# Kernel optimization log

Measured on AMD Instinct MI355X. Metric: run time of the kernel, lower is better.

Reference implementation:

```python
import jax, jax.numpy as jnp
import numpy as np

K = 3            # TAGConv default number of hops
NUM_GRAPHS = 128 # graphs in the batch (for global_add_pool)


def _gcn_norm(src, dst, n):
    # PyG gcn_norm (symmetric, no self-loops): w_e = d[src]^-1/2 * d[dst]^-1/2
    deg = jnp.zeros((n,), jnp.float32).at[dst].add(1.0)
    dinv = jnp.where(deg > 0, jax.lax.rsqrt(deg), 0.0)
    return dinv[src] * dinv[dst]


def _tagconv(x, src, dst, wn, W, b):
    # out = sum_{k=0..K} (norm_adj^k x) @ W[k] + b
    n = x.shape[0]
    h = x
    out = h @ W[0]
    for k in range(1, K + 1):
        h = jax.ops.segment_sum(h[src] * wn[:, None], dst, num_segments=n)
        out = out + h @ W[k]
    return out + b


def setup_inputs() -> dict:
    key = jax.random.key(0)
    ks = jax.random.split(key, 8)
    N, E, D, H = 50000, 800000, 64, 64
    x = jax.random.normal(ks[0], (N, D), jnp.float32)
    edge_index = jax.random.randint(ks[1], (2, E), 0, N, dtype=jnp.int32)
    batch_ids = jnp.sort(jax.random.randint(ks[2], (N,), 0, NUM_GRAPHS, dtype=jnp.int32))
    def glorot(k, sh):
        return jax.random.normal(k, sh, jnp.float32) / np.float32(np.sqrt(sh[-2]))
    W0 = glorot(ks[3], (K + 1, D, H)); b0 = jnp.zeros((H,), jnp.float32)
    W1 = glorot(ks[4], (K + 1, H, H)); b1 = jnp.zeros((H,), jnp.float32)
    alpha0 = jnp.full((1,), 0.25, jnp.float32)  # PReLU default init
    alpha1 = jnp.full((1,), 0.25, jnp.float32)
    Wout = glorot(ks[5], (H, 1)); bout = jnp.zeros((1,), jnp.float32)
    return dict(x=x, edge_index=edge_index, batch_ids=batch_ids,
                W0=W0, b0=b0, W1=W1, b1=b1,
                alpha0=alpha0, alpha1=alpha1, Wout=Wout, bout=bout)


def reference(x, edge_index, batch_ids, W0, b0, W1, b1, alpha0, alpha1, Wout, bout):
    src, dst = edge_index[0], edge_index[1]
    wn = _gcn_norm(src, dst, x.shape[0])
    # layer 0: TAGConv -> (dropout=identity in eval) -> PReLU
    h = _tagconv(x, src, dst, wn, W0, b0)
    h = jnp.where(h >= 0, h, alpha0 * h)
    # layer 1
    h = _tagconv(h, src, dst, wn, W1, b1)
    h = jnp.where(h >= 0, h, alpha1 * h)
    # global_add_pool over graphs, then linear critic head
    g = jax.ops.segment_sum(h, batch_ids, num_segments=NUM_GRAPHS)  # [G, H]
    return g @ Wout + bout  # [G, 1]
```

## Files before the change

kernel.cpp:

```cpp
#include <hip/hip_runtime.h>
#include <hip/hip_bf16.h>
#include <hip/hip_fp16.h>

#define D 64
#define GRAPHS 128

using bf16x8 = __attribute__((ext_vector_type(8))) short;
using f32x4  = __attribute__((ext_vector_type(4))) float;


__device__ __forceinline__ float bf2f(unsigned short u) {
    return __uint_as_float(((unsigned)u) << 16);
}
__device__ __forceinline__ unsigned short f2bf(float f) {
    unsigned u = __float_as_uint(f);
    unsigned r = (u + 0x7FFFu + ((u >> 16) & 1u)) >> 16;
    return (unsigned short)r;
}


__global__ void deg_prep_kernel(const int* __restrict__ dst, int* __restrict__ deg,
                                int* __restrict__ pos, int E, int EB4,
                                const float* __restrict__ W0, const float* __restrict__ W1,
                                unsigned short* __restrict__ WF0, unsigned short* __restrict__ WF1,
                                const float* __restrict__ x, unsigned short* __restrict__ H, int NH) {
    int b = blockIdx.x;
    if (b < EB4) {
        int e0 = (b * 256 + threadIdx.x) * 4;
        if (e0 + 4 <= E) {
            int4 d4 = *(const int4*)(dst + e0);
            int4 p;
            p.x = atomicAdd(&deg[d4.x], 1);
            p.y = atomicAdd(&deg[d4.y], 1);
            p.z = atomicAdd(&deg[d4.z], 1);
            p.w = atomicAdd(&deg[d4.w], 1);
            *(int4*)(pos + e0) = p;
        } else {
            for (int e = e0; e < E; ++e) pos[e] = atomicAdd(&deg[dst[e]], 1);
        }
    } else if (b < EB4 + 128) {
        int idx = (b - EB4) * 256 + threadIdx.x;
        int i = idx & 16383;
        int j = i & 7, lane = (i >> 3) & 63, ct = (i >> 9) & 3, kt = i >> 11;
        int n = ct * 16 + (lane & 15);
        int k = kt * 32 + (lane >> 4) * 8 + j;
        if (idx < 16384) WF0[i] = f2bf(W0[k * 64 + n]);
        else             WF1[i] = f2bf(W1[k * 64 + n]);
    } else {
        int i = (b - EB4 - 128) * 256 + threadIdx.x;
        if (i < NH) {
            int n = i >> 3, f = (i & 7) * 8;
            float4 x0 = *(const float4*)(x + (size_t)n * 64 + f);
            float4 x1 = *(const float4*)(x + (size_t)n * 64 + f + 4);
            bf16x8 pk;
            pk[0] = f2bf(x0.x); pk[1] = f2bf(x0.y); pk[2] = f2bf(x0.z); pk[3] = f2bf(x0.w);
            pk[4] = f2bf(x1.x); pk[5] = f2bf(x1.y); pk[6] = f2bf(x1.z); pk[7] = f2bf(x1.w);
            *(bf16x8*)(H + (size_t)n * 256 + f) = pk;
        }
    }
}


__global__ void scan_all_kernel(const int* __restrict__ deg, float* __restrict__ dinv,
                                int* __restrict__ pdeg, int* __restrict__ rowstart,
                                unsigned int* __restrict__ ep, int* __restrict__ total, int N) {
    __shared__ int s[256];
    __shared__ int base_sh;
    int i = blockIdx.x * 256 + threadIdx.x;
    int d = 0, p = 0;
    if (i < N) {
        d = deg[i];
        dinv[i] = d > 0 ? rsqrtf((float)d) : 0.0f;
        p = (d + 7) & ~7;
        pdeg[i] = p;
    }
    s[threadIdx.x] = p;
    __syncthreads();
    for (int st = 1; st < 256; st <<= 1) {
        int add = (threadIdx.x >= st) ? s[threadIdx.x - st] : 0;
        __syncthreads();
        s[threadIdx.x] += add;
        __syncthreads();
    }
    if (threadIdx.x == 255) base_sh = atomicAdd(total, s[255]);
    __syncthreads();
    if (i < N) {
        int excl = base_sh + s[threadIdx.x] - p;
        rowstart[i] = excl;
        for (int q = excl + d; q < excl + p; ++q) ep[q] = 0u;
    }
}


__global__ void scatter_kernel(const int* __restrict__ src, const int* __restrict__ dst,
                               const int* __restrict__ pos, const float* __restrict__ dinv,
                               const int* __restrict__ rowstart, unsigned int* __restrict__ ep, int E) {
    int e0 = (blockIdx.x * 256 + threadIdx.x) * 4;
    if (e0 + 4 <= E) {
        int4 s4 = *(const int4*)(src + e0);
        int4 d4 = *(const int4*)(dst + e0);
        int4 p4 = *(const int4*)(pos + e0);
        float v0 = dinv[s4.x], v1 = dinv[s4.y], v2 = dinv[s4.z], v3 = dinv[s4.w];
        int r0 = rowstart[d4.x], r1 = rowstart[d4.y], r2 = rowstart[d4.z], r3 = rowstart[d4.w];
        ep[r0 + p4.x] = (unsigned)s4.x | ((unsigned)__half_as_ushort(__float2half(v0)) << 16);
        ep[r1 + p4.y] = (unsigned)s4.y | ((unsigned)__half_as_ushort(__float2half(v1)) << 16);
        ep[r2 + p4.z] = (unsigned)s4.z | ((unsigned)__half_as_ushort(__float2half(v2)) << 16);
        ep[r3 + p4.w] = (unsigned)s4.w | ((unsigned)__half_as_ushort(__float2half(v3)) << 16);
    } else {
        for (int e = e0; e < E; ++e) {
            int dd = dst[e], ss = src[e];
            ep[rowstart[dd] + pos[e]] = (unsigned)ss | ((unsigned)__half_as_ushort(__float2half(dinv[ss])) << 16);
        }
    }
}


#define GROWS 8

__global__ __launch_bounds__(512, 8)
void gather_kernel(const unsigned short* __restrict__ in,
                   unsigned short* __restrict__ out,
                   const int* __restrict__ rowstart, const int* __restrict__ pdeg,
                   const float* __restrict__ dinv, const unsigned int* __restrict__ ep, int N) {
    int wid = blockIdx.x * GROWS + (threadIdx.x >> 6);
    if (wid >= N) return;
    int lane = threadIdx.x & 63;
    int g  = lane >> 3;
    int fl = (lane & 7) * 8;

    int start = __builtin_amdgcn_readfirstlane(rowstart[wid]);
    int cnt   = __builtin_amdgcn_readfirstlane(pdeg[wid]);
    float dd  = dinv[wid];

    float a0=0.f,a1=0.f,a2=0.f,a3=0.f,a4=0.f,a5=0.f,a6=0.f,a7=0.f;
    float c0=0.f,c1=0.f,c2=0.f,c3=0.f,c4=0.f,c5=0.f,c6=0.f,c7=0.f;
    unsigned eA = 0, eB = 0;
    if (cnt > 0) {
        eA = ep[start + g];
        eB = (8 < cnt) ? ep[start + 8 + g] : 0u;
    }
    for (int i = 0; i < cnt; i += 16) {
        unsigned cA = eA, cB = eB;
        if (i + 16 < cnt) {
            eA = ep[start + i + 16 + g];
            eB = (i + 24 < cnt) ? ep[start + i + 24 + g] : 0u;
        }
        bf16x8 rA = *(const bf16x8*)(in + (size_t)(cA & 0xFFFFu) * 256 + fl);
        bf16x8 rB = *(const bf16x8*)(in + (size_t)(cB & 0xFFFFu) * 256 + fl);
        float wA = __half2float(__ushort_as_half((unsigned short)(cA >> 16)));
        float wB = __half2float(__ushort_as_half((unsigned short)(cB >> 16)));
        a0 = fmaf(wA, bf2f((unsigned short)rA[0]), a0);
        a1 = fmaf(wA, bf2f((unsigned short)rA[1]), a1);
        a2 = fmaf(wA, bf2f((unsigned short)rA[2]), a2);
        a3 = fmaf(wA, bf2f((unsigned short)rA[3]), a3);
        a4 = fmaf(wA, bf2f((unsigned short)rA[4]), a4);
        a5 = fmaf(wA, bf2f((unsigned short)rA[5]), a5);
        a6 = fmaf(wA, bf2f((unsigned short)rA[6]), a6);
        a7 = fmaf(wA, bf2f((unsigned short)rA[7]), a7);
        c0 = fmaf(wB, bf2f((unsigned short)rB[0]), c0);
        c1 = fmaf(wB, bf2f((unsigned short)rB[1]), c1);
        c2 = fmaf(wB, bf2f((unsigned short)rB[2]), c2);
        c3 = fmaf(wB, bf2f((unsigned short)rB[3]), c3);
        c4 = fmaf(wB, bf2f((unsigned short)rB[4]), c4);
        c5 = fmaf(wB, bf2f((unsigned short)rB[5]), c5);
        c6 = fmaf(wB, bf2f((unsigned short)rB[6]), c6);
        c7 = fmaf(wB, bf2f((unsigned short)rB[7]), c7);
    }
    a0 += c0; a1 += c1; a2 += c2; a3 += c3;
    a4 += c4; a5 += c5; a6 += c6; a7 += c7;
    a0 += __shfl_xor(a0, 8, 64); a0 += __shfl_xor(a0, 16, 64); a0 += __shfl_xor(a0, 32, 64);
    a1 += __shfl_xor(a1, 8, 64); a1 += __shfl_xor(a1, 16, 64); a1 += __shfl_xor(a1, 32, 64);
    a2 += __shfl_xor(a2, 8, 64); a2 += __shfl_xor(a2, 16, 64); a2 += __shfl_xor(a2, 32, 64);
    a3 += __shfl_xor(a3, 8, 64); a3 += __shfl_xor(a3, 16, 64); a3 += __shfl_xor(a3, 32, 64);
    a4 += __shfl_xor(a4, 8, 64); a4 += __shfl_xor(a4, 16, 64); a4 += __shfl_xor(a4, 32, 64);
    a5 += __shfl_xor(a5, 8, 64); a5 += __shfl_xor(a5, 16, 64); a5 += __shfl_xor(a5, 32, 64);
    a6 += __shfl_xor(a6, 8, 64); a6 += __shfl_xor(a6, 16, 64); a6 += __shfl_xor(a6, 32, 64);
    a7 += __shfl_xor(a7, 8, 64); a7 += __shfl_xor(a7, 16, 64); a7 += __shfl_xor(a7, 32, 64);
    if (g == 0) {
        bf16x8 pk;
        pk[0] = f2bf(a0 * dd); pk[1] = f2bf(a1 * dd);
        pk[2] = f2bf(a2 * dd); pk[3] = f2bf(a3 * dd);
        pk[4] = f2bf(a4 * dd); pk[5] = f2bf(a5 * dd);
        pk[6] = f2bf(a6 * dd); pk[7] = f2bf(a7 * dd);
        *(bf16x8*)(out + (size_t)wid * 256 + fl) = pk;
    }
}


#define LROW 72

template<int MODE>
__global__ __launch_bounds__(256, 4)
void tag_gemm_kernel(const unsigned short* __restrict__ H,
                     const unsigned short* __restrict__ Wfrag,
                     const float* __restrict__ bias, const float* __restrict__ alpha,
                     const float* __restrict__ Wout, const int* __restrict__ batch,
                     const float* __restrict__ bout,
                     unsigned short* __restrict__ H2, float* __restrict__ outp, int N) {
    __shared__ float bins[GRAPHS];
    __shared__ unsigned short lbuf[64 * LROW];
    if (MODE == 3) {
        if (threadIdx.x < GRAPHS) bins[threadIdx.x] = 0.0f;
        __syncthreads();
    }
    if (MODE == 2) {
        if (blockIdx.x == 0 && threadIdx.x < GRAPHS) outp[threadIdx.x] = bout[0];
    }

    int w = threadIdx.x >> 6, lane = threadIdx.x & 63;
    int m = lane & 15, quad = lane >> 4;
    int rowbase = blockIdx.x * 64 + w * 16;
    int arow = rowbase + m;
    size_t aoff = (size_t)min(arow, N - 1) * 256 + quad * 8;

    f32x4 acc0 = {0.f, 0.f, 0.f, 0.f}, acc1 = acc0, acc2 = acc0, acc3 = acc0;
#pragma unroll
    for (int kt = 0; kt < 8; ++kt) {
        bf16x8 A = *(const bf16x8*)(H + aoff + kt * 32);
        const unsigned short* wf = Wfrag + ((size_t)(kt * 4) * 64 + lane) * 8;
        bf16x8 B0 = *(const bf16x8*)(wf + 0 * 64 * 8);
        bf16x8 B1 = *(const bf16x8*)(wf + 1 * 64 * 8);
        bf16x8 B2 = *(const bf16x8*)(wf + 2 * 64 * 8);
        bf16x8 B3 = *(const bf16x8*)(wf + 3 * 64 * 8);
        acc0 = __builtin_amdgcn_mfma_f32_16x16x32_bf16(A, B0, acc0, 0, 0, 0);
        acc1 = __builtin_amdgcn_mfma_f32_16x16x32_bf16(A, B1, acc1, 0, 0, 0);
        acc2 = __builtin_amdgcn_mfma_f32_16x16x32_bf16(A, B2, acc2, 0, 0, 0);
        acc3 = __builtin_amdgcn_mfma_f32_16x16x32_bf16(A, B3, acc3, 0, 0, 0);
    }

    float al = alpha[0];
    f32x4 accs[4] = {acc0, acc1, acc2, acc3};
    if (MODE == 2) {
#pragma unroll
        for (int ct = 0; ct < 4; ++ct) {
            int col = ct * 16 + m;
            float b = bias[col];
#pragma unroll
            for (int r = 0; r < 4; ++r) {
                int lrow = w * 16 + quad * 4 + r;
                float v = accs[ct][r] + b;
                v = v >= 0.f ? v : al * v;
                lbuf[lrow * LROW + col] = f2bf(v);
            }
        }
        __syncthreads();
#pragma unroll
        for (int k = 0; k < 2; ++k) {
            int c = threadIdx.x * 2 + k;
            int lrow = c >> 3, part = c & 7;
            int grow = blockIdx.x * 64 + lrow;
            if (grow < N) {
                bf16x8 pk = *(const bf16x8*)(lbuf + lrow * LROW + part * 8);
                *(bf16x8*)(H2 + (size_t)grow * 256 + part * 8) = pk;
            }
        }
    } else {
        float rv0 = 0.f, rv1 = 0.f, rv2 = 0.f, rv3 = 0.f;
#pragma unroll
        for (int ct = 0; ct < 4; ++ct) {
            int col = ct * 16 + m;
            float b = bias[col], wo = Wout[col];
            float v;
            v = accs[ct][0] + b; v = v >= 0.f ? v : al * v; rv0 = fmaf(v, wo, rv0);
            v = accs[ct][1] + b; v = v >= 0.f ? v : al * v; rv1 = fmaf(v, wo, rv1);
            v = accs[ct][2] + b; v = v >= 0.f ? v : al * v; rv2 = fmaf(v, wo, rv2);
            v = accs[ct][3] + b; v = v >= 0.f ? v : al * v; rv3 = fmaf(v, wo, rv3);
        }
        float rv[4] = {rv0, rv1, rv2, rv3};
#pragma unroll
        for (int r = 0; r < 4; ++r) {
            float v = rv[r];
            v += __shfl_xor(v, 8, 16);
            v += __shfl_xor(v, 4, 16);
            v += __shfl_xor(v, 2, 16);
            v += __shfl_xor(v, 1, 16);
            int row = rowbase + quad * 4 + r;
            if (m == 0 && row < N) atomicAdd(&bins[batch[row]], v);
        }
        __syncthreads();
        if (threadIdx.x < GRAPHS) {
            float bv = bins[threadIdx.x];
            if (bv != 0.0f) atomicAdd(&outp[threadIdx.x], bv);
        }
    }
}

extern "C" void kernel_launch(void* const* d_in, const int* in_sizes, int n_in,
                              void* d_out, int out_size, void* d_ws, size_t ws_size,
                              hipStream_t stream) {
    const float* x     = (const float*)d_in[0];
    const int*   ei    = (const int*)d_in[1];
    const int*   batch = (const int*)d_in[2];
    const float* W0    = (const float*)d_in[3];
    const float* b0    = (const float*)d_in[4];
    const float* W1    = (const float*)d_in[5];
    const float* b1    = (const float*)d_in[6];
    const float* a0    = (const float*)d_in[7];
    const float* a1    = (const float*)d_in[8];
    const float* Wout  = (const float*)d_in[9];
    const float* bout  = (const float*)d_in[10];

    const int N = in_sizes[0] / D;
    const int E = in_sizes[1] / 2;
    const int* src = ei;
    const int* dst = ei + E;

    size_t off = 0;
    auto alloc = [&](size_t bytes) -> void* {
        void* p = (char*)d_ws + off;
        off = (off + bytes + 255) & ~(size_t)255;
        return p;
    };
    const int NB = (N + 255) / 256;
    int*   deg      = (int*)alloc((size_t)(N + 1) * 4);
    int*   pdeg     = (int*)alloc((size_t)N * 4);
    int*   rowstart = (int*)alloc((size_t)N * 4);
    float* dinv     = (float*)alloc((size_t)N * 4);
    int*   pos      = (int*)alloc((size_t)E * 4);
    unsigned int* epack = (unsigned int*)alloc(((size_t)E + 8ull * N) * 4);
    unsigned short* HA = (unsigned short*)alloc((size_t)N * 256 * 2);
    unsigned short* HB = (unsigned short*)alloc((size_t)N * 256 * 2);
    unsigned short* WF0 = (unsigned short*)alloc(16384 * 2);
    unsigned short* WF1 = (unsigned short*)alloc(16384 * 2);

    const int EB4 = (E + 1023) / 1024;
    const int NXH = (N * 8 + 255) / 256;
    const int NG = (N + GROWS - 1) / GROWS;
    const int NM = (N + 63) / 64;

    hipMemsetAsync(deg, 0, (size_t)(N + 1) * 4, stream);
    deg_prep_kernel<<<EB4 + 128 + NXH, 256, 0, stream>>>(dst, deg, pos, E, EB4,
                                                         W0, W1, WF0, WF1, x, HA, N * 8);
    scan_all_kernel<<<NB, 256, 0, stream>>>(deg, dinv, pdeg, rowstart, epack, deg + N, N);
    scatter_kernel<<<EB4, 256, 0, stream>>>(src, dst, pos, dinv, rowstart, epack, E);

    gather_kernel<<<NG, 512, 0, stream>>>(HA + 0 * 64, HA + 1 * 64, rowstart, pdeg, dinv, epack, N);
    gather_kernel<<<NG, 512, 0, stream>>>(HA + 1 * 64, HA + 2 * 64, rowstart, pdeg, dinv, epack, N);
    gather_kernel<<<NG, 512, 0, stream>>>(HA + 2 * 64, HA + 3 * 64, rowstart, pdeg, dinv, epack, N);
    tag_gemm_kernel<2><<<NM, 256, 0, stream>>>(HA, WF0, b0, a0, nullptr, nullptr, bout,
                                               HB, (float*)d_out, N);

    gather_kernel<<<NG, 512, 0, stream>>>(HB + 0 * 64, HB + 1 * 64, rowstart, pdeg, dinv, epack, N);
    gather_kernel<<<NG, 512, 0, stream>>>(HB + 1 * 64, HB + 2 * 64, rowstart, pdeg, dinv, epack, N);
    gather_kernel<<<NG, 512, 0, stream>>>(HB + 2 * 64, HB + 3 * 64, rowstart, pdeg, dinv, epack, N);
    tag_gemm_kernel<3><<<NM, 256, 0, stream>>>(HB, WF1, b1, a1, Wout, batch, bout,
                                               nullptr, (float*)d_out, N);
}
```

Baseline: 276.5 us.

## Split feature planes into 32-wide halves and gather each half separately

Features move from one interleaved [N,256] bf16 buffer to eight separate [N,32] planes. Each hop now runs as two gather passes over 32-feature halves, so the randomly gathered working set per pass is half as large and can stay in cache better. The gather also uses nontemporal loads for edges and nontemporal stores for outputs, drops the dual-accumulator unroll, and adds one more shuffle-reduction stage. The cost is twice as many gather launches, with the edge list read twice per hop.

```diff
diff --git a/kernel.cpp b/kernel.cpp
--- a/kernel.cpp
+++ b/kernel.cpp
@@ -17,6 +17,7 @@
     unsigned r = (u + 0x7FFFu + ((u >> 16) & 1u)) >> 16;
     return (unsigned short)r;
 }
+
 
 
 __global__ void deg_prep_kernel(const int* __restrict__ dst, int* __restrict__ deg,
@@ -49,13 +50,14 @@
     } else {
         int i = (b - EB4 - 128) * 256 + threadIdx.x;
         if (i < NH) {
-            int n = i >> 3, f = (i & 7) * 8;
-            float4 x0 = *(const float4*)(x + (size_t)n * 64 + f);
-            float4 x1 = *(const float4*)(x + (size_t)n * 64 + f + 4);
+            int n = i >> 3, part = i & 7;
+            size_t HS = (size_t)NH * 4;
+            float4 x0 = *(const float4*)(x + (size_t)n * 64 + part * 8);
+            float4 x1 = *(const float4*)(x + (size_t)n * 64 + part * 8 + 4);
             bf16x8 pk;
             pk[0] = f2bf(x0.x); pk[1] = f2bf(x0.y); pk[2] = f2bf(x0.z); pk[3] = f2bf(x0.w);
             pk[4] = f2bf(x1.x); pk[5] = f2bf(x1.y); pk[6] = f2bf(x1.z); pk[7] = f2bf(x1.w);
-            *(bf16x8*)(H + (size_t)n * 256 + f) = pk;
+            *(bf16x8*)(H + (size_t)(part >> 2) * HS + (size_t)n * 32 + (part & 3) * 8) = pk;
         }
     }
 }
@@ -118,37 +120,30 @@
 #define GROWS 8
 
 __global__ __launch_bounds__(512, 8)
-void gather_kernel(const unsigned short* __restrict__ in,
-                   unsigned short* __restrict__ out,
-                   const int* __restrict__ rowstart, const int* __restrict__ pdeg,
-                   const float* __restrict__ dinv, const unsigned int* __restrict__ ep, int N) {
+void gather_half_kernel(const unsigned short* __restrict__ in,
+                        unsigned short* __restrict__ out,
+                        const int* __restrict__ rowstart, const int* __restrict__ pdeg,
+                        const float* __restrict__ dinv, const unsigned int* __restrict__ ep, int N) {
     int wid = blockIdx.x * GROWS + (threadIdx.x >> 6);
     if (wid >= N) return;
     int lane = threadIdx.x & 63;
-    int g  = lane >> 3;
-    int fl = (lane & 7) * 8;
+    int g  = lane >> 2;
+    int fl = (lane & 3) * 8;
 
     int start = __builtin_amdgcn_readfirstlane(rowstart[wid]);
     int cnt   = __builtin_amdgcn_readfirstlane(pdeg[wid]);
     float dd  = dinv[wid];
 
     float a0=0.f,a1=0.f,a2=0.f,a3=0.f,a4=0.f,a5=0.f,a6=0.f,a7=0.f;
-    float c0=0.f,c1=0.f,c2=0.f,c3=0.f,c4=0.f,c5=0.f,c6=0.f,c7=0.f;
-    unsigned eA = 0, eB = 0;
-    if (cnt > 0) {
-        eA = ep[start + g];
-        eB = (8 < cnt) ? ep[start + 8 + g] : 0u;
-    }
+    unsigned eA = 0;
+    if (cnt > 0)
+        eA = (g < cnt) ? __builtin_nontemporal_load(ep + start + g) : 0u;
     for (int i = 0; i < cnt; i += 16) {
-        unsigned cA = eA, cB = eB;
-        if (i + 16 < cnt) {
-            eA = ep[start + i + 16 + g];
-            eB = (i + 24 < cnt) ? ep[start + i + 24 + g] : 0u;
-        }
-        bf16x8 rA = *(const bf16x8*)(in + (size_t)(cA & 0xFFFFu) * 256 + fl);
-        bf16x8 rB = *(const bf16x8*)(in + (size_t)(cB & 0xFFFFu) * 256 + fl);
+        unsigned cA = eA;
+        if (i + 16 < cnt)
+            eA = (i + 16 + g < cnt) ? __builtin_nontemporal_load(ep + start + i + 16 + g) : 0u;
+        bf16x8 rA = *(const bf16x8*)(in + (size_t)(cA & 0xFFFFu) * 32 + fl);
         float wA = __half2float(__ushort_as_half((unsigned short)(cA >> 16)));
-        float wB = __half2float(__ushort_as_half((unsigned short)(cB >> 16)));
         a0 = fmaf(wA, bf2f((unsigned short)rA[0]), a0);
         a1 = fmaf(wA, bf2f((unsigned short)rA[1]), a1);
         a2 = fmaf(wA, bf2f((unsigned short)rA[2]), a2);
@@ -157,32 +152,22 @@
         a5 = fmaf(wA, bf2f((unsigned short)rA[5]), a5);
         a6 = fmaf(wA, bf2f((unsigned short)rA[6]), a6);
         a7 = fmaf(wA, bf2f((unsigned short)rA[7]), a7);
-        c0 = fmaf(wB, bf2f((unsigned short)rB[0]), c0);
-        c1 = fmaf(wB, bf2f((unsigned short)rB[1]), c1);
-        c2 = fmaf(wB, bf2f((unsigned short)rB[2]), c2);
-        c3 = fmaf(wB, bf2f((unsigned short)rB[3]), c3);
-        c4 = fmaf(wB, bf2f((unsigned short)rB[4]), c4);
-        c5 = fmaf(wB, bf2f((unsigned short)rB[5]), c5);
-        c6 = fmaf(wB, bf2f((unsigned short)rB[6]), c6);
-        c7 = fmaf(wB, bf2f((unsigned short)rB[7]), c7);
-    }
-    a0 += c0; a1 += c1; a2 += c2; a3 += c3;
-    a4 += c4; a5 += c5; a6 += c6; a7 += c7;
-    a0 += __shfl_xor(a0, 8, 64); a0 += __shfl_xor(a0, 16, 64); a0 += __shfl_xor(a0, 32, 64);
-    a1 += __shfl_xor(a1, 8, 64); a1 += __shfl_xor(a1, 16, 64); a1 += __shfl_xor(a1, 32, 64);
-    a2 += __shfl_xor(a2, 8, 64); a2 += __shfl_xor(a2, 16, 64); a2 += __shfl_xor(a2, 32, 64);
-    a3 += __shfl_xor(a3, 8, 64); a3 += __shfl_xor(a3, 16, 64); a3 += __shfl_xor(a3, 32, 64);
-    a4 += __shfl_xor(a4, 8, 64); a4 += __shfl_xor(a4, 16, 64); a4 += __shfl_xor(a4, 32, 64);
-    a5 += __shfl_xor(a5, 8, 64); a5 += __shfl_xor(a5, 16, 64); a5 += __shfl_xor(a5, 32, 64);
-    a6 += __shfl_xor(a6, 8, 64); a6 += __shfl_xor(a6, 16, 64); a6 += __shfl_xor(a6, 32, 64);
-    a7 += __shfl_xor(a7, 8, 64); a7 += __shfl_xor(a7, 16, 64); a7 += __shfl_xor(a7, 32, 64);
+    }
+    a0 += __shfl_xor(a0, 4, 64); a0 += __shfl_xor(a0, 8, 64); a0 += __shfl_xor(a0, 16, 64); a0 += __shfl_xor(a0, 32, 64);
+    a1 += __shfl_xor(a1, 4, 64); a1 += __shfl_xor(a1, 8, 64); a1 += __shfl_xor(a1, 16, 64); a1 += __shfl_xor(a1, 32, 64);
+    a2 += __shfl_xor(a2, 4, 64); a2 += __shfl_xor(a2, 8, 64); a2 += __shfl_xor(a2, 16, 64); a2 += __shfl_xor(a2, 32, 64);
+    a3 += __shfl_xor(a3, 4, 64); a3 += __shfl_xor(a3, 8, 64); a3 += __shfl_xor(a3, 16, 64); a3 += __shfl_xor(a3, 32, 64);
+    a4 += __shfl_xor(a4, 4, 64); a4 += __shfl_xor(a4, 8, 64); a4 += __shfl_xor(a4, 16, 64); a4 += __shfl_xor(a4, 32, 64);
+    a5 += __shfl_xor(a5, 4, 64); a5 += __shfl_xor(a5, 8, 64); a5 += __shfl_xor(a5, 16, 64); a5 += __shfl_xor(a5, 32, 64);
+    a6 += __shfl_xor(a6, 4, 64); a6 += __shfl_xor(a6, 8, 64); a6 += __shfl_xor(a6, 16, 64); a6 += __shfl_xor(a6, 32, 64);
+    a7 += __shfl_xor(a7, 4, 64); a7 += __shfl_xor(a7, 8, 64); a7 += __shfl_xor(a7, 16, 64); a7 += __shfl_xor(a7, 32, 64);
     if (g == 0) {
         bf16x8 pk;
         pk[0] = f2bf(a0 * dd); pk[1] = f2bf(a1 * dd);
         pk[2] = f2bf(a2 * dd); pk[3] = f2bf(a3 * dd);
         pk[4] = f2bf(a4 * dd); pk[5] = f2bf(a5 * dd);
         pk[6] = f2bf(a6 * dd); pk[7] = f2bf(a7 * dd);
-        *(bf16x8*)(out + (size_t)wid * 256 + fl) = pk;
+        __builtin_nontemporal_store(pk, (bf16x8*)(out + (size_t)wid * 32 + fl));
     }
 }
 
@@ -211,12 +196,13 @@
     int m = lane & 15, quad = lane >> 4;
     int rowbase = blockIdx.x * 64 + w * 16;
     int arow = rowbase + m;
-    size_t aoff = (size_t)min(arow, N - 1) * 256 + quad * 8;
+    size_t HS = (size_t)N * 32;
+    const unsigned short* abase = H + (size_t)min(arow, N - 1) * 32 + quad * 8;
 
     f32x4 acc0 = {0.f, 0.f, 0.f, 0.f}, acc1 = acc0, acc2 = acc0, acc3 = acc0;
 #pragma unroll
     for (int kt = 0; kt < 8; ++kt) {
-        bf16x8 A = *(const bf16x8*)(H + aoff + kt * 32);
+        bf16x8 A = *(const bf16x8*)(abase + (size_t)kt * HS);
         const unsigned short* wf = Wfrag + ((size_t)(kt * 4) * 64 + lane) * 8;
         bf16x8 B0 = *(const bf16x8*)(wf + 0 * 64 * 8);
         bf16x8 B1 = *(const bf16x8*)(wf + 1 * 64 * 8);
@@ -251,7 +237,7 @@
             int grow = blockIdx.x * 64 + lrow;
             if (grow < N) {
                 bf16x8 pk = *(const bf16x8*)(lbuf + lrow * LROW + part * 8);
-                *(bf16x8*)(H2 + (size_t)grow * 256 + part * 8) = pk;
+                *(bf16x8*)(H2 + (size_t)(part >> 2) * HS + (size_t)grow * 32 + (part & 3) * 8) = pk;
             }
         }
     } else {
@@ -323,6 +309,7 @@
     unsigned short* WF0 = (unsigned short*)alloc(16384 * 2);
     unsigned short* WF1 = (unsigned short*)alloc(16384 * 2);
 
+    const size_t HS = (size_t)N * 32;
     const int EB4 = (E + 1023) / 1024;
     const int NXH = (N * 8 + 255) / 256;
     const int NG = (N + GROWS - 1) / GROWS;
@@ -334,15 +321,25 @@
     scan_all_kernel<<<NB, 256, 0, stream>>>(deg, dinv, pdeg, rowstart, epack, deg + N, N);
     scatter_kernel<<<EB4, 256, 0, stream>>>(src, dst, pos, dinv, rowstart, epack, E);
 
-    gather_kernel<<<NG, 512, 0, stream>>>(HA + 0 * 64, HA + 1 * 64, rowstart, pdeg, dinv, epack, N);
-    gather_kernel<<<NG, 512, 0, stream>>>(HA + 1 * 64, HA + 2 * 64, rowstart, pdeg, dinv, epack, N);
-    gather_kernel<<<NG, 512, 0, stream>>>(HA + 2 * 64, HA + 3 * 64, rowstart, pdeg, dinv, epack, N);
+    for (int hop = 1; hop <= 3; ++hop) {
+        gather_half_kernel<<<NG, 512, 0, stream>>>(HA + (size_t)((hop - 1) * 2 + 0) * HS,
+                                                   HA + (size_t)(hop * 2 + 0) * HS,
+                                                   rowstart, pdeg, dinv, epack, N);
+        gather_half_kernel<<<NG, 512, 0, stream>>>(HA + (size_t)((hop - 1) * 2 + 1) * HS,
+                                                   HA + (size_t)(hop * 2 + 1) * HS,
+                                                   rowstart, pdeg, dinv, epack, N);
+    }
     tag_gemm_kernel<2><<<NM, 256, 0, stream>>>(HA, WF0, b0, a0, nullptr, nullptr, bout,
                                                HB, (float*)d_out, N);
 
-    gather_kernel<<<NG, 512, 0, stream>>>(HB + 0 * 64, HB + 1 * 64, rowstart, pdeg, dinv, epack, N);
-    gather_kernel<<<NG, 512, 0, stream>>>(HB + 1 * 64, HB + 2 * 64, rowstart, pdeg, dinv, epack, N);
-    gather_kernel<<<NG, 512, 0, stream>>>(HB + 2 * 64, HB + 3 * 64, rowstart, pdeg, dinv, epack, N);
+    for (int hop = 1; hop <= 3; ++hop) {
+        gather_half_kernel<<<NG, 512, 0, stream>>>(HB + (size_t)((hop - 1) * 2 + 0) * HS,
+                                                   HB + (size_t)(hop * 2 + 0) * HS,
+                                                   rowstart, pdeg, dinv, epack, N);
+        gather_half_kernel<<<NG, 512, 0, stream>>>(HB + (size_t)((hop - 1) * 2 + 1) * HS,
+                                                   HB + (size_t)(hop * 2 + 1) * HS,
+                                                   rowstart, pdeg, dinv, epack, N);
+    }
     tag_gemm_kernel<3><<<NM, 256, 0, stream>>>(HB, WF1, b1, a1, Wout, batch, bout,
                                                nullptr, (float*)d_out, N);
 }
```

New measurement: 410.3 us. 48.4% more time.

## Build CSR via two-pass LSD radix bucketing instead of global atomic counting

Applied to the files above, without the earlier changes.

Replaces per-edge global atomics on a degree array with a two-level radix sort on destination. Edges are first bucketed into 256 coarse groups using shared-memory histograms and per-block cursor reservation, then sorted within each group by the low 8 bits in shared memory, which also produces degrees, row starts and dinv. Edge weights are filled in a separate pass. The aim is to cut global atomic contention and scattered writes. In exchange, rows are no longer padded to multiples of 8, so the gather kernel now bounds-checks each lane's edge load, and the pipeline gains extra kernel launches and a temporary buffer.

```diff
diff --git a/kernel.cpp b/kernel.cpp
--- a/kernel.cpp
+++ b/kernel.cpp
@@ -19,27 +19,28 @@
 }
 
 
-__global__ void deg_prep_kernel(const int* __restrict__ dst, int* __restrict__ deg,
-                                int* __restrict__ pos, int E, int EB4,
-                                const float* __restrict__ W0, const float* __restrict__ W1,
-                                unsigned short* __restrict__ WF0, unsigned short* __restrict__ WF1,
-                                const float* __restrict__ x, unsigned short* __restrict__ H, int NH) {
+
+__global__ void prep_kernel(const int* __restrict__ dst, int* __restrict__ gcount,
+                            int E, int B1,
+                            const float* __restrict__ W0, const float* __restrict__ W1,
+                            unsigned short* __restrict__ WF0, unsigned short* __restrict__ WF1,
+                            const float* __restrict__ x, unsigned short* __restrict__ H, int NH) {
     int b = blockIdx.x;
-    if (b < EB4) {
-        int e0 = (b * 256 + threadIdx.x) * 4;
-        if (e0 + 4 <= E) {
-            int4 d4 = *(const int4*)(dst + e0);
-            int4 p;
-            p.x = atomicAdd(&deg[d4.x], 1);
-            p.y = atomicAdd(&deg[d4.y], 1);
-            p.z = atomicAdd(&deg[d4.z], 1);
-            p.w = atomicAdd(&deg[d4.w], 1);
-            *(int4*)(pos + e0) = p;
-        } else {
-            for (int e = e0; e < E; ++e) pos[e] = atomicAdd(&deg[dst[e]], 1);
-        }
-    } else if (b < EB4 + 128) {
-        int idx = (b - EB4) * 256 + threadIdx.x;
+    if (b < B1) {
+        __shared__ int hist[256];
+        int t = threadIdx.x;
+        hist[t] = 0;
+        __syncthreads();
+        int e0 = b * 2048 + t;
+#pragma unroll
+        for (int r = 0; r < 8; ++r) {
+            int e = e0 + r * 256;
+            if (e < E) atomicAdd(&hist[dst[e] >> 8], 1);
+        }
+        __syncthreads();
+        if (hist[t]) atomicAdd(&gcount[t * 32], hist[t]);
+    } else if (b < B1 + 128) {
+        int idx = (b - B1) * 256 + threadIdx.x;
         int i = idx & 16383;
         int j = i & 7, lane = (i >> 3) & 63, ct = (i >> 9) & 3, kt = i >> 11;
         int n = ct * 16 + (lane & 15);
@@ -47,7 +48,7 @@
         if (idx < 16384) WF0[i] = f2bf(W0[k * 64 + n]);
         else             WF1[i] = f2bf(W1[k * 64 + n]);
     } else {
-        int i = (b - EB4 - 128) * 256 + threadIdx.x;
+        int i = (b - B1 - 128) * 256 + threadIdx.x;
         if (i < NH) {
             int n = i >> 3, f = (i & 7) * 8;
             float4 x0 = *(const float4*)(x + (size_t)n * 64 + f);
@@ -61,55 +62,121 @@
 }
 
 
-__global__ void scan_all_kernel(const int* __restrict__ deg, float* __restrict__ dinv,
-                                int* __restrict__ pdeg, int* __restrict__ rowstart,
-                                unsigned int* __restrict__ ep, int* __restrict__ total, int N) {
+__global__ void scan256_kernel(const int* __restrict__ gcount, int* __restrict__ gbase,
+                               int* __restrict__ gcursor, int E) {
     __shared__ int s[256];
-    __shared__ int base_sh;
-    int i = blockIdx.x * 256 + threadIdx.x;
-    int d = 0, p = 0;
-    if (i < N) {
-        d = deg[i];
-        dinv[i] = d > 0 ? rsqrtf((float)d) : 0.0f;
-        p = (d + 7) & ~7;
-        pdeg[i] = p;
-    }
-    s[threadIdx.x] = p;
+    int t = threadIdx.x;
+    int c = gcount[t * 32];
+    s[t] = c;
     __syncthreads();
     for (int st = 1; st < 256; st <<= 1) {
-        int add = (threadIdx.x >= st) ? s[threadIdx.x - st] : 0;
-        __syncthreads();
-        s[threadIdx.x] += add;
-        __syncthreads();
-    }
-    if (threadIdx.x == 255) base_sh = atomicAdd(total, s[255]);
-    __syncthreads();
-    if (i < N) {
-        int excl = base_sh + s[threadIdx.x] - p;
-        rowstart[i] = excl;
-        for (int q = excl + d; q < excl + p; ++q) ep[q] = 0u;
-    }
-}
-
-
-__global__ void scatter_kernel(const int* __restrict__ src, const int* __restrict__ dst,
-                               const int* __restrict__ pos, const float* __restrict__ dinv,
-                               const int* __restrict__ rowstart, unsigned int* __restrict__ ep, int E) {
+        int add = (t >= st) ? s[t - st] : 0;
+        __syncthreads();
+        s[t] += add;
+        __syncthreads();
+    }
+    int excl = s[t] - c;
+    gbase[t] = excl;
+    gcursor[t * 32] = excl;
+    if (t == 255) gbase[256] = E;
+}
+
+
+__global__ void bucket_kernel(const int* __restrict__ dst, const int* __restrict__ src,
+                              int* __restrict__ gcursor, unsigned int* __restrict__ tmp32, int E) {
+    __shared__ int hist[256];
+    __shared__ int basec[256];
+    int t = threadIdx.x, b = blockIdx.x;
+    hist[t] = 0;
+    __syncthreads();
+    unsigned pk[8];
+    int bk[8];
+    int e0 = b * 2048 + t;
+#pragma unroll
+    for (int r = 0; r < 8; ++r) {
+        int e = e0 + r * 256;
+        if (e < E) {
+            int d = dst[e];
+            pk[r] = ((unsigned)d << 16) | (unsigned)src[e];
+            bk[r] = d >> 8;
+            atomicAdd(&hist[bk[r]], 1);
+        } else bk[r] = -1;
+    }
+    __syncthreads();
+    if (hist[t]) basec[t] = atomicAdd(&gcursor[t * 32], hist[t]);
+    __syncthreads();
+#pragma unroll
+    for (int r = 0; r < 8; ++r) {
+        if (bk[r] >= 0) {
+            int slot = atomicAdd(&basec[bk[r]], 1);
+            tmp32[slot] = pk[r];
+        }
+    }
+}
+
+
+__global__ __launch_bounds__(512)
+void radix2_kernel(const int* __restrict__ gbase, const unsigned int* __restrict__ tmp32,
+                   unsigned int* __restrict__ ep, float* __restrict__ dinv,
+                   int* __restrict__ pdeg, int* __restrict__ rowstart, int N) {
+    __shared__ int s[256];
+    __shared__ int hist[256];
+    __shared__ int cur[256];
+    int h = blockIdx.x, t = threadIdx.x;
+    int start = gbase[h];
+    int cnt   = gbase[h + 1] - start;
+
+    if (t < 256) hist[t] = 0;
+    __syncthreads();
+    for (int j = t; j < cnt; j += 512)
+        atomicAdd(&hist[(tmp32[start + j] >> 16) & 0xFF], 1);
+    __syncthreads();
+
+    int myc = (t < 256) ? hist[t] : 0;
+    if (t < 256) s[t] = myc;
+    __syncthreads();
+    for (int st = 1; st < 256; st <<= 1) {
+        int add = (t < 256 && t >= st) ? s[t - st] : 0;
+        __syncthreads();
+        if (t < 256) s[t] += add;
+        __syncthreads();
+    }
+    if (t < 256) {
+        int excl = s[t] - myc;
+        int node = h * 256 + t;
+        if (node < N) {
+            pdeg[node] = myc;
+            rowstart[node] = start + excl;
+            dinv[node] = myc > 0 ? rsqrtf((float)myc) : 0.0f;
+        }
+        cur[t] = excl;
+    }
+    __syncthreads();
+
+    for (int j = t; j < cnt; j += 512) {
+        unsigned v = tmp32[start + j];
+        int lo = (v >> 16) & 0xFF;
+        int r = atomicAdd(&cur[lo], 1);
+        ep[start + r] = v & 0xFFFFu;
+    }
+}
+
+
+__global__ void wfix_kernel(unsigned int* __restrict__ ep, const float* __restrict__ dinv, int E) {
     int e0 = (blockIdx.x * 256 + threadIdx.x) * 4;
     if (e0 + 4 <= E) {
-        int4 s4 = *(const int4*)(src + e0);
-        int4 d4 = *(const int4*)(dst + e0);
-        int4 p4 = *(const int4*)(pos + e0);
-        float v0 = dinv[s4.x], v1 = dinv[s4.y], v2 = dinv[s4.z], v3 = dinv[s4.w];
-        int r0 = rowstart[d4.x], r1 = rowstart[d4.y], r2 = rowstart[d4.z], r3 = rowstart[d4.w];
-        ep[r0 + p4.x] = (unsigned)s4.x | ((unsigned)__half_as_ushort(__float2half(v0)) << 16);
-        ep[r1 + p4.y] = (unsigned)s4.y | ((unsigned)__half_as_ushort(__float2half(v1)) << 16);
-        ep[r2 + p4.z] = (unsigned)s4.z | ((unsigned)__half_as_ushort(__float2half(v2)) << 16);
-        ep[r3 + p4.w] = (unsigned)s4.w | ((unsigned)__half_as_ushort(__float2half(v3)) << 16);
+        uint4 v = *(const uint4*)(ep + e0);
+        unsigned w0 = __half_as_ushort(__float2half(dinv[v.x]));
+        unsigned w1 = __half_as_ushort(__float2half(dinv[v.y]));
+        unsigned w2 = __half_as_ushort(__float2half(dinv[v.z]));
+        unsigned w3 = __half_as_ushort(__float2half(dinv[v.w]));
+        v.x |= w0 << 16; v.y |= w1 << 16; v.z |= w2 << 16; v.w |= w3 << 16;
+        *(uint4*)(ep + e0) = v;
     } else {
         for (int e = e0; e < E; ++e) {
-            int dd = dst[e], ss = src[e];
-            ep[rowstart[dd] + pos[e]] = (unsigned)ss | ((unsigned)__half_as_ushort(__float2half(dinv[ss])) << 16);
+            unsigned v = ep[e];
+            v |= (unsigned)__half_as_ushort(__float2half(dinv[v])) << 16;
+            ep[e] = v;
         }
     }
 }
@@ -136,14 +203,14 @@
     float c0=0.f,c1=0.f,c2=0.f,c3=0.f,c4=0.f,c5=0.f,c6=0.f,c7=0.f;
     unsigned eA = 0, eB = 0;
     if (cnt > 0) {
-        eA = ep[start + g];
-        eB = (8 < cnt) ? ep[start + 8 + g] : 0u;
+        eA = (g < cnt) ? ep[start + g] : 0u;
+        eB = (8 + g < cnt) ? ep[start + 8 + g] : 0u;
     }
     for (int i = 0; i < cnt; i += 16) {
         unsigned cA = eA, cB = eB;
         if (i + 16 < cnt) {
-            eA = ep[start + i + 16 + g];
-            eB = (i + 24 < cnt) ? ep[start + i + 24 + g] : 0u;
+            eA = (i + 16 + g < cnt) ? ep[start + i + 16 + g] : 0u;
+            eB = (i + 24 + g < cnt) ? ep[start + i + 24 + g] : 0u;
         }
         bf16x8 rA = *(const bf16x8*)(in + (size_t)(cA & 0xFFFFu) * 256 + fl);
         bf16x8 rB = *(const bf16x8*)(in + (size_t)(cB & 0xFFFFu) * 256 + fl);
@@ -311,28 +378,33 @@
         off = (off + bytes + 255) & ~(size_t)255;
         return p;
     };
-    const int NB = (N + 255) / 256;
-    int*   deg      = (int*)alloc((size_t)(N + 1) * 4);
+    int*   gcount   = (int*)alloc(256 * 32 * 4);
+    int*   gcursor  = (int*)alloc(256 * 32 * 4);
+    int*   gbase    = (int*)alloc(257 * 4);
     int*   pdeg     = (int*)alloc((size_t)N * 4);
     int*   rowstart = (int*)alloc((size_t)N * 4);
     float* dinv     = (float*)alloc((size_t)N * 4);
-    int*   pos      = (int*)alloc((size_t)E * 4);
-    unsigned int* epack = (unsigned int*)alloc(((size_t)E + 8ull * N) * 4);
+    unsigned int* tmp32 = (unsigned int*)alloc((size_t)E * 4);
+    unsigned int* epack = (unsigned int*)alloc((size_t)E * 4);
     unsigned short* HA = (unsigned short*)alloc((size_t)N * 256 * 2);
     unsigned short* HB = (unsigned short*)alloc((size_t)N * 256 * 2);
     unsigned short* WF0 = (unsigned short*)alloc(16384 * 2);
     unsigned short* WF1 = (unsigned short*)alloc(16384 * 2);
 
+    const int B1  = (E + 2047) / 2048;
+    const int NXH = (N * 8 + 255) / 256;
+    const int NH256 = (N + 255) / 256;
     const int EB4 = (E + 1023) / 1024;
-    const int NXH = (N * 8 + 255) / 256;
     const int NG = (N + GROWS - 1) / GROWS;
     const int NM = (N + 63) / 64;
 
-    hipMemsetAsync(deg, 0, (size_t)(N + 1) * 4, stream);
-    deg_prep_kernel<<<EB4 + 128 + NXH, 256, 0, stream>>>(dst, deg, pos, E, EB4,
-                                                         W0, W1, WF0, WF1, x, HA, N * 8);
-    scan_all_kernel<<<NB, 256, 0, stream>>>(deg, dinv, pdeg, rowstart, epack, deg + N, N);
-    scatter_kernel<<<EB4, 256, 0, stream>>>(src, dst, pos, dinv, rowstart, epack, E);
+    hipMemsetAsync(gcount, 0, 256 * 32 * 4, stream);
+    prep_kernel<<<B1 + 128 + NXH, 256, 0, stream>>>(dst, gcount, E, B1,
+                                                    W0, W1, WF0, WF1, x, HA, N * 8);
+    scan256_kernel<<<1, 256, 0, stream>>>(gcount, gbase, gcursor, E);
+    bucket_kernel<<<B1, 256, 0, stream>>>(dst, src, gcursor, tmp32, E);
+    radix2_kernel<<<NH256, 512, 0, stream>>>(gbase, tmp32, epack, dinv, pdeg, rowstart, N);
+    wfix_kernel<<<EB4, 256, 0, stream>>>(epack, dinv, E);
 
     gather_kernel<<<NG, 512, 0, stream>>>(HA + 0 * 64, HA + 1 * 64, rowstart, pdeg, dinv, epack, N);
     gather_kernel<<<NG, 512, 0, stream>>>(HA + 1 * 64, HA + 2 * 64, rowstart, pdeg, dinv, epack, N);
```

New measurement: 258.5 us, median of 2. 6.5% less time.
